# Kernel tuning notes

Hardware: AMD Instinct MI355X
Metric: run time of the kernel (lower is better)

The kernel has to match this reference:

```python
import jax, jax.numpy as jnp
import numpy as np

B, S, D = 32, 128, 1024      # encoder batch, seq len, embed_dim
C = 65536                    # nclasses (sense inventory)
N = 512                      # number of gathered WSD target tokens
NNZ = 262144                 # nnz of sparse label adjacency A (avg degree 4)
EPS = 1e-5                   # BatchNorm1d eps


def setup_inputs() -> dict:
    key = jax.random.key(0)
    ks = jax.random.split(key, 7)
    enc_out = jax.random.normal(ks[0], (B, S, D), dtype=jnp.float32)
    batch_idx = jax.random.randint(ks[1], (N,), 0, B)
    tgt = jax.random.randint(ks[2], (N,), 0, S)
    A_indices = jax.random.randint(ks[3], (2, NNZ), 0, C)
    A_values = jax.random.uniform(ks[4], (NNZ,), dtype=jnp.float32)
    wt2_w = jax.random.normal(ks[5], (C, D), dtype=jnp.float32) / np.sqrt(D).astype(np.float32)
    wt2_b = jax.random.normal(ks[6], (C,), dtype=jnp.float32) * 0.02
    return {"enc_out": enc_out, "wt2_w": wt2_w, "wt2_b": wt2_b,
            "A_values": A_values, "batch_idx": batch_idx, "tgt": tgt,
            "A_indices": A_indices}


def reference(enc_out, wt2_w, wt2_b, A_values, batch_idx, tgt, A_indices):
    # gather target-token embeddings: [N, D]
    g = enc_out[batch_idx, tgt]
    # BatchNorm1d(affine=False), training mode -> batch stats, biased var
    mean = jnp.mean(g, axis=0)
    var = jnp.var(g, axis=0)
    h0 = (g - mean) / jnp.sqrt(var + EPS)
    # wt2 Linear + swish -> logits over classes Z: [N, C]
    h1 = jax.nn.swish(h0 @ wt2_w.T + wt2_b)
    # sparse spmm: torch_sparse.spmm(ii, vv, m=C, n=C, matrix=Z.T).T == Z @ A.T
    row, col = A_indices[0], A_indices[1]
    gathered = h1.T[col] * A_values[:, None]            # [NNZ, N]
    neighbors = jax.ops.segment_sum(gathered, row, num_segments=C).T  # [N, C]
    # residual add (renormalize=False)
    return neighbors + h1
```

## Files before the change

### kernel.cpp

```cpp
#include <hip/hip_runtime.h>
#include <hip/hip_bf16.h>

typedef unsigned short u16;
typedef unsigned int   u32;
typedef __attribute__((ext_vector_type(8))) short bf16x8;
typedef __attribute__((ext_vector_type(4))) float f32x4;

static constexpr int kS = 128, kD = 1024, kC = 65536, kN = 512, kNNZ = 262144;

__device__ __forceinline__ u16 f2bf(float x) {
  u32 u = __float_as_uint(x);
  u32 r = (u + 0x7fffu + ((u >> 16) & 1u)) >> 16;
  return (u16)r;
}
__device__ __forceinline__ u32 pack2(float a, float b) {
  return (u32)f2bf(a) | ((u32)f2bf(b) << 16);
}
__device__ __forceinline__ float bf_lo(u32 v) { return __uint_as_float(v << 16); }
__device__ __forceinline__ float bf_hi(u32 v) { return __uint_as_float(v & 0xffff0000u); }

__global__ void k_bn_part(const float* __restrict__ enc, const int* __restrict__ bidx,
                          const int* __restrict__ tgt, float* __restrict__ part) {
  __shared__ int offs[64];
  int n0 = blockIdx.y * 64;
  if (threadIdx.x < 64) offs[threadIdx.x] = bidx[n0 + threadIdx.x] * kS + tgt[n0 + threadIdx.x];
  __syncthreads();
  int d = blockIdx.x * 256 + threadIdx.x;
  float s = 0.f, ss = 0.f;
  for (int i = 0; i < 64; ++i) {
    float v = enc[(size_t)offs[i] * kD + d];
    s += v; ss += v * v;
  }
  part[(blockIdx.y * 2 + 0) * kD + d] = s;
  part[(blockIdx.y * 2 + 1) * kD + d] = ss;
}

__global__ void k_bn_fin(const float* __restrict__ part, float* __restrict__ mean,
                         float* __restrict__ rstd) {
  int d = blockIdx.x * 256 + threadIdx.x;
  float s = 0.f, ss = 0.f;
#pragma unroll
  for (int b = 0; b < 8; ++b) {
    s  += part[(b * 2 + 0) * kD + d];
    ss += part[(b * 2 + 1) * kD + d];
  }
  float m = s * (1.f / kN);
  float var = ss * (1.f / kN) - m * m;
  mean[d] = m;
  rstd[d] = 1.f / sqrtf(var + 1e-5f);
}

__global__ void k_bn_apply(const float* __restrict__ enc, const int* __restrict__ bidx,
                           const int* __restrict__ tgt, const float* __restrict__ mean,
                           const float* __restrict__ rstd, u16* __restrict__ h0) {
  int i = blockIdx.x * blockDim.x + threadIdx.x;
  int n = i >> 8;
  int d = (i & 255) << 2;
  size_t src = (size_t)(bidx[n] * kS + tgt[n]) * kD + d;
  float4 v  = *(const float4*)(enc + src);
  float4 mn = *(const float4*)(mean + d);
  float4 rs = *(const float4*)(rstd + d);
  u32 q0 = pack2((v.x - mn.x) * rs.x, (v.y - mn.y) * rs.y);
  u32 q1 = pack2((v.z - mn.z) * rs.z, (v.w - mn.w) * rs.w);
  *(uint2*)(h0 + (size_t)n * kD + d) = make_uint2(q0, q1);
}

__global__ void k_hist(const int* __restrict__ rows, int* __restrict__ hist) {
  int e = blockIdx.x * blockDim.x + threadIdx.x;
  if (e < kNNZ) atomicAdd(&hist[rows[e]], 1);
}

__global__ __launch_bounds__(1024) void k_scan(int* __restrict__ hist, int* __restrict__ cursor) {
  __shared__ int sm[1024];
  int t = threadIdx.x;
  int base = t * 64;
  int sum = 0;
  for (int i = 0; i < 64; ++i) sum += hist[base + i];
  sm[t] = sum;
  __syncthreads();
  for (int off = 1; off < 1024; off <<= 1) {
    int v = (t >= off) ? sm[t - off] : 0;
    __syncthreads();
    sm[t] += v;
    __syncthreads();
  }
  int run = sm[t] - sum;
  for (int i = 0; i < 64; ++i) {
    int v = hist[base + i];
    hist[base + i] = run;
    cursor[base + i] = run;
    run += v;
  }
  if (t == 1023) hist[kC] = run;
}

__global__ void k_scatter(const int* __restrict__ rows, const int* __restrict__ cols,
                          const float* __restrict__ vals, int* __restrict__ cursor,
                          int* __restrict__ scol, float* __restrict__ sval) {
  int e = blockIdx.x * blockDim.x + threadIdx.x;
  if (e < kNNZ) {
    int r = rows[e];
    int p = atomicAdd(&cursor[r], 1);
    scol[p] = cols[e];
    sval[p] = vals[e];
  }
}

__global__ __launch_bounds__(512)
void k_gemm_f(const float* __restrict__ W, const u16* __restrict__ h0,
              const float* __restrict__ bias, u16* __restrict__ h1t) {
  __shared__ __align__(16) u16 Ab[128 * 40];
  __shared__ __align__(16) u16 Bb[512 * 40];
  const int t = threadIdx.x;
  const int l = t & 63, w = t >> 6;
  const int wm = (w >> 2) * 64, wn = (w & 3) * 128;
  const int cb = blockIdx.x * 128;

  const int ar = t >> 3, aq = t & 7;
  const int br = t >> 2, bq = t & 3;

  const float* gA0 = W + (size_t)(cb + ar) * kD + aq * 4;
  const float* gA1 = W + (size_t)(cb + ar + 64) * kD + aq * 4;
  const u16*   gB  = h0 + (size_t)br * kD + bq * 8;

  char* Abc = (char*)Ab;
  char* Bbc = (char*)Bb;
  u32 aw0 = ar * 80 + aq * 8, aw1 = (ar + 64) * 80 + aq * 8;
  u32 bw = br * 80 + bq * 16;

  f32x4 acc[4][8];
#pragma unroll
  for (int a = 0; a < 4; ++a)
#pragma unroll
    for (int b = 0; b < 8; ++b) acc[a][b] = (f32x4){0.f, 0.f, 0.f, 0.f};

  float4 nA0 = *(const float4*)gA0;
  float4 nA1 = *(const float4*)gA1;
  uint4 nB0 = *(const uint4*)(gB);
  uint4 nB1 = *(const uint4*)(gB + 128 * kD);
  uint4 nB2 = *(const uint4*)(gB + 256 * kD);
  uint4 nB3 = *(const uint4*)(gB + 384 * kD);

#pragma unroll 1
  for (int it = 0; it < 32; ++it) {
    *(uint2*)(Abc + aw0) = make_uint2(pack2(nA0.x, nA0.y), pack2(nA0.z, nA0.w));
    *(uint2*)(Abc + aw1) = make_uint2(pack2(nA1.x, nA1.y), pack2(nA1.z, nA1.w));
    *(uint4*)(Bbc + bw)  = nB0;
    *(uint4*)(Bbc + bw + 128 * 80) = nB1;
    *(uint4*)(Bbc + bw + 256 * 80) = nB2;
    *(uint4*)(Bbc + bw + 384 * 80) = nB3;
    int ktn = (it < 31) ? (it + 1) * 32 : 0;
    nA0 = *(const float4*)(gA0 + ktn);
    nA1 = *(const float4*)(gA1 + ktn);
    nB0 = *(const uint4*)(gB + ktn);
    nB1 = *(const uint4*)(gB + 128 * kD + ktn);
    nB2 = *(const uint4*)(gB + 256 * kD + ktn);
    nB3 = *(const uint4*)(gB + 384 * kD + ktn);
    asm volatile("s_waitcnt lgkmcnt(0)" ::: "memory");
    __builtin_amdgcn_s_barrier();
    __builtin_amdgcn_sched_barrier(0);
    bf16x8 af[4], bv[8];
#pragma unroll
    for (int mb = 0; mb < 4; ++mb)
      af[mb] = *(const bf16x8*)(Abc + (wm + mb * 16 + (l & 15)) * 80 + (l >> 4) * 16);
#pragma unroll
    for (int nb = 0; nb < 8; ++nb)
      bv[nb] = *(const bf16x8*)(Bbc + (wn + nb * 16 + (l & 15)) * 80 + (l >> 4) * 16);
#pragma unroll
    for (int mb = 0; mb < 4; ++mb)
#pragma unroll
      for (int nb = 0; nb < 8; ++nb)
        acc[mb][nb] = __builtin_amdgcn_mfma_f32_16x16x32_bf16(af[mb], bv[nb], acc[mb][nb], 0, 0, 0);
    asm volatile("s_waitcnt lgkmcnt(0)" ::: "memory");
    __builtin_amdgcn_s_barrier();
    __builtin_amdgcn_sched_barrier(0);
  }

#pragma unroll
  for (int mb = 0; mb < 4; ++mb) {
    int rb = wm + mb * 16 + (l >> 4) * 4;
#pragma unroll
    for (int i = 0; i < 4; ++i) {
      int c = cb + rb + i;
      float bvs = bias[c];
#pragma unroll
      for (int nb = 0; nb < 8; ++nb) {
        float x = acc[mb][nb][i] + bvs;
        float sw = x / (1.f + __expf(-x));
        h1t[(size_t)c * kN + (wn + nb * 16 + (l & 15))] = f2bf(sw);
      }
    }
  }
}

__global__ __launch_bounds__(512)
void k_spmm(const u16* __restrict__ h1t, const int* __restrict__ rowptr,
            const int* __restrict__ scol, const float* __restrict__ sval,
            float* __restrict__ out) {
  __shared__ float tile[32 * 512];
  int r0 = blockIdx.x * 32;
  int t = threadIdx.x, w = t >> 6, l = t & 63;
#pragma unroll
  for (int j = 0; j < 4; ++j) {
    int rl = w * 4 + j;
    int r = r0 + rl;
    uint4 hv = ((const uint4*)(h1t + (size_t)r * kN))[l];
    float a0 = bf_lo(hv.x), a1 = bf_hi(hv.x), a2 = bf_lo(hv.y), a3 = bf_hi(hv.y);
    float a4 = bf_lo(hv.z), a5 = bf_hi(hv.z), a6 = bf_lo(hv.w), a7 = bf_hi(hv.w);
    int e0 = rowptr[r], e1 = rowptr[r + 1];
    int c = 0; float v = 0.f;
    if (e0 < e1) { c = scol[e0]; v = sval[e0]; }
    for (int e = e0; e < e1; ++e) {
      uint4 cv = ((const uint4*)(h1t + (size_t)c * kN))[l];
      int cn = 0; float vn = 0.f;
      if (e + 1 < e1) { cn = scol[e + 1]; vn = sval[e + 1]; }
      a0 = fmaf(v, bf_lo(cv.x), a0); a1 = fmaf(v, bf_hi(cv.x), a1);
      a2 = fmaf(v, bf_lo(cv.y), a2); a3 = fmaf(v, bf_hi(cv.y), a3);
      a4 = fmaf(v, bf_lo(cv.z), a4); a5 = fmaf(v, bf_hi(cv.z), a5);
      a6 = fmaf(v, bf_lo(cv.w), a6); a7 = fmaf(v, bf_hi(cv.w), a7);
      c = cn; v = vn;
    }
    int sw = (rl & 7) << 2;
    *(float4*)&tile[rl * 512 + ((8 * l) ^ sw)]     = make_float4(a0, a1, a2, a3);
    *(float4*)&tile[rl * 512 + ((8 * l + 4) ^ sw)] = make_float4(a4, a5, a6, a7);
  }
  __syncthreads();
  int r = l & 31;
  int swr = (r & 7) << 2;
#pragma unroll
  for (int it = 0; it < 32; ++it) {
    int n = it * 16 + w * 2 + (l >> 5);
    out[(size_t)n * kC + r0 + r] = tile[r * 512 + (n ^ swr)];
  }
}

extern "C" void kernel_launch(void* const* d_in, const int* in_sizes, int n_in,
                              void* d_out, int out_size, void* d_ws, size_t ws_size,
                              hipStream_t stream) {
  (void)in_sizes; (void)n_in; (void)out_size; (void)ws_size;
  const float* enc   = (const float*)d_in[0];
  const float* W     = (const float*)d_in[1];
  const float* bias  = (const float*)d_in[2];
  const float* Avals = (const float*)d_in[3];
  const int*   bidx  = (const int*)d_in[4];
  const int*   tgt   = (const int*)d_in[5];
  const int*   Arow  = (const int*)d_in[6];
  const int*   Acol  = Arow + kNNZ;
  float* out = (float*)d_out;

  char* ws = (char*)d_ws;
  float* mean   = (float*)(ws);
  float* rstd   = (float*)(ws + 4096);
  u16*   h0     = (u16*)  (ws + 8192);
  int*   rowptr = (int*)  (ws + 1056768);
  int*   cursor = (int*)  (ws + 1319168);
  int*   scol   = (int*)  (ws + 1581312);
  float* sval   = (float*)(ws + 2629888);
  float* part   = (float*)(ws + 3678464);
  u16*   h1t    = (u16*)  (ws + 4194304);

  hipMemsetAsync(rowptr, 0, (kC + 1) * sizeof(int), stream);
  k_bn_part<<<dim3(4, 8), 256, 0, stream>>>(enc, bidx, tgt, part);
  k_bn_fin<<<4, 256, 0, stream>>>(part, mean, rstd);
  k_bn_apply<<<512, 256, 0, stream>>>(enc, bidx, tgt, mean, rstd, h0);
  k_hist<<<kNNZ / 256, 256, 0, stream>>>(Arow, rowptr);
  k_scan<<<1, 1024, 0, stream>>>(rowptr, cursor);
  k_scatter<<<kNNZ / 256, 256, 0, stream>>>(Arow, Acol, Avals, cursor, scol, sval);
  k_gemm_f<<<kC / 128, 512, 0, stream>>>(W, h0, bias, h1t);
  k_spmm<<<kC / 32, 512, 0, stream>>>(h1t, rowptr, scol, sval, out);
}
```

Measured before the change: 293.9 us.

## Pre-pack activations in MFMA fragment layout and load B operand directly from global

The BN apply kernel now writes the normalized activations in a k-group-major packed layout, so each lane of the GEMM can load its B-operand MFMA fragment straight from global memory into registers instead of staging it through LDS. The GEMM moves to 1024 threads with a 2x8 wave grid of 64x64 tiles and double-buffers the small W tile in LDS across alternating k-steps. This cuts LDS traffic and LDS footprint. In exchange every wave re-reads B from global or L2, and the larger block raises register pressure.

```diff
diff --git a/kernel.cpp b/kernel.cpp
--- a/kernel.cpp
+++ b/kernel.cpp
@@ -50,19 +50,25 @@
   rstd[d] = 1.f / sqrtf(var + 1e-5f);
 }
 
-__global__ void k_bn_apply(const float* __restrict__ enc, const int* __restrict__ bidx,
-                           const int* __restrict__ tgt, const float* __restrict__ mean,
-                           const float* __restrict__ rstd, u16* __restrict__ h0) {
-  int i = blockIdx.x * blockDim.x + threadIdx.x;
-  int n = i >> 8;
-  int d = (i & 255) << 2;
-  size_t src = (size_t)(bidx[n] * kS + tgt[n]) * kD + d;
-  float4 v  = *(const float4*)(enc + src);
-  float4 mn = *(const float4*)(mean + d);
-  float4 rs = *(const float4*)(rstd + d);
-  u32 q0 = pack2((v.x - mn.x) * rs.x, (v.y - mn.y) * rs.y);
-  u32 q1 = pack2((v.z - mn.z) * rs.z, (v.w - mn.w) * rs.w);
-  *(uint2*)(h0 + (size_t)n * kD + d) = make_uint2(q0, q1);
+__global__ void k_bn_pack(const float* __restrict__ enc, const int* __restrict__ bidx,
+                          const int* __restrict__ tgt, const float* __restrict__ mean,
+                          const float* __restrict__ rstd, u16* __restrict__ Bp) {
+  int i = blockIdx.x * 256 + threadIdx.x;
+  int n = i & 511;
+  int g = i >> 9;
+  int k0 = g * 8;
+  size_t src = (size_t)(bidx[n] * kS + tgt[n]) * kD + k0;
+  float4 v0 = *(const float4*)(enc + src);
+  float4 v1 = *(const float4*)(enc + src + 4);
+  float4 m0 = *(const float4*)(mean + k0);
+  float4 m1 = *(const float4*)(mean + k0 + 4);
+  float4 r0 = *(const float4*)(rstd + k0);
+  float4 r1 = *(const float4*)(rstd + k0 + 4);
+  u32 q0 = pack2((v0.x - m0.x) * r0.x, (v0.y - m0.y) * r0.y);
+  u32 q1 = pack2((v0.z - m0.z) * r0.z, (v0.w - m0.w) * r0.w);
+  u32 q2 = pack2((v1.x - m1.x) * r1.x, (v1.y - m1.y) * r1.y);
+  u32 q3 = pack2((v1.z - m1.z) * r1.z, (v1.w - m1.w) * r1.w);
+  *(uint4*)(Bp + (size_t)i * 8) = make_uint4(q0, q1, q2, q3);
 }
 
 __global__ void k_hist(const int* __restrict__ rows, int* __restrict__ hist) {
@@ -106,88 +112,97 @@
   }
 }
 
-__global__ __launch_bounds__(512)
-void k_gemm_f(const float* __restrict__ W, const u16* __restrict__ h0,
-              const float* __restrict__ bias, u16* __restrict__ h1t) {
-  __shared__ __align__(16) u16 Ab[128 * 40];
-  __shared__ __align__(16) u16 Bb[512 * 40];
+__global__ __launch_bounds__(1024)
+void k_gemm_f2(const float* __restrict__ W, const u16* __restrict__ Bp,
+               const float* __restrict__ bias, u16* __restrict__ h1t) {
+  __shared__ __align__(16) u16 Ab0[128 * 36];
+  __shared__ __align__(16) u16 Ab1[128 * 36];
   const int t = threadIdx.x;
-  const int l = t & 63, w = t >> 6;
-  const int wm = (w >> 2) * 64, wn = (w & 3) * 128;
+  const int l = t & 63;
+  const int w = t >> 6;
+  const int wm = (w >> 3) * 64, wn = (w & 7) * 64;
   const int cb = blockIdx.x * 128;
-
   const int ar = t >> 3, aq = t & 7;
-  const int br = t >> 2, bq = t & 3;
-
-  const float* gA0 = W + (size_t)(cb + ar) * kD + aq * 4;
-  const float* gA1 = W + (size_t)(cb + ar + 64) * kD + aq * 4;
-  const u16*   gB  = h0 + (size_t)br * kD + bq * 8;
-
-  char* Abc = (char*)Ab;
-  char* Bbc = (char*)Bb;
-  u32 aw0 = ar * 80 + aq * 8, aw1 = (ar + 64) * 80 + aq * 8;
-  u32 bw = br * 80 + bq * 16;
-
-  f32x4 acc[4][8];
+  const int q = l >> 4, ln = l & 15;
+  const float* gA = W + (size_t)(cb + ar) * kD + aq * 4;
+  u16* awp0 = Ab0 + ar * 36 + aq * 4;
+  u16* awp1 = Ab1 + ar * 36 + aq * 4;
+  const u16* gB = Bp + ((size_t)q * 512 + wn + ln) * 8;
+
+  f32x4 acc[4][4];
 #pragma unroll
   for (int a = 0; a < 4; ++a)
 #pragma unroll
-    for (int b = 0; b < 8; ++b) acc[a][b] = (f32x4){0.f, 0.f, 0.f, 0.f};
-
-  float4 nA0 = *(const float4*)gA0;
-  float4 nA1 = *(const float4*)gA1;
-  uint4 nB0 = *(const uint4*)(gB);
-  uint4 nB1 = *(const uint4*)(gB + 128 * kD);
-  uint4 nB2 = *(const uint4*)(gB + 256 * kD);
-  uint4 nB3 = *(const uint4*)(gB + 384 * kD);
+    for (int b = 0; b < 4; ++b) acc[a][b] = (f32x4){0.f, 0.f, 0.f, 0.f};
+
+  float4 fA;
+  bf16x8 bvA[4], bvB[4];
+
+  fA = *(const float4*)(gA);
+#pragma unroll
+  for (int nb = 0; nb < 4; ++nb) bvA[nb] = *(const bf16x8*)(gB + nb * 128);
+  *(uint2*)awp0 = make_uint2(pack2(fA.x, fA.y), pack2(fA.z, fA.w));
+  fA = *(const float4*)(gA + 32);
+#pragma unroll
+  for (int nb = 0; nb < 4; ++nb) bvB[nb] = *(const bf16x8*)(gB + 16384 + nb * 128);
+  asm volatile("s_waitcnt lgkmcnt(0)" ::: "memory");
+  __builtin_amdgcn_s_barrier();
+  __builtin_amdgcn_sched_barrier(0);
 
 #pragma unroll 1
-  for (int it = 0; it < 32; ++it) {
-    *(uint2*)(Abc + aw0) = make_uint2(pack2(nA0.x, nA0.y), pack2(nA0.z, nA0.w));
-    *(uint2*)(Abc + aw1) = make_uint2(pack2(nA1.x, nA1.y), pack2(nA1.z, nA1.w));
-    *(uint4*)(Bbc + bw)  = nB0;
-    *(uint4*)(Bbc + bw + 128 * 80) = nB1;
-    *(uint4*)(Bbc + bw + 256 * 80) = nB2;
-    *(uint4*)(Bbc + bw + 384 * 80) = nB3;
-    int ktn = (it < 31) ? (it + 1) * 32 : 0;
-    nA0 = *(const float4*)(gA0 + ktn);
-    nA1 = *(const float4*)(gA1 + ktn);
-    nB0 = *(const uint4*)(gB + ktn);
-    nB1 = *(const uint4*)(gB + 128 * kD + ktn);
-    nB2 = *(const uint4*)(gB + 256 * kD + ktn);
-    nB3 = *(const uint4*)(gB + 384 * kD + ktn);
-    asm volatile("s_waitcnt lgkmcnt(0)" ::: "memory");
-    __builtin_amdgcn_s_barrier();
-    __builtin_amdgcn_sched_barrier(0);
-    bf16x8 af[4], bv[8];
-#pragma unroll
-    for (int mb = 0; mb < 4; ++mb)
-      af[mb] = *(const bf16x8*)(Abc + (wm + mb * 16 + (l & 15)) * 80 + (l >> 4) * 16);
-#pragma unroll
-    for (int nb = 0; nb < 8; ++nb)
-      bv[nb] = *(const bf16x8*)(Bbc + (wn + nb * 16 + (l & 15)) * 80 + (l >> 4) * 16);
-#pragma unroll
-    for (int mb = 0; mb < 4; ++mb)
-#pragma unroll
-      for (int nb = 0; nb < 8; ++nb)
-        acc[mb][nb] = __builtin_amdgcn_mfma_f32_16x16x32_bf16(af[mb], bv[nb], acc[mb][nb], 0, 0, 0);
-    asm volatile("s_waitcnt lgkmcnt(0)" ::: "memory");
-    __builtin_amdgcn_s_barrier();
-    __builtin_amdgcn_sched_barrier(0);
+  for (int tt = 0; tt < 16; ++tt) {
+    {
+#pragma unroll
+      for (int mb = 0; mb < 4; ++mb) {
+        bf16x8 af = *(const bf16x8*)(Ab0 + (wm + mb * 16 + ln) * 36 + q * 8);
+#pragma unroll
+        for (int nb = 0; nb < 4; ++nb)
+          acc[mb][nb] = __builtin_amdgcn_mfma_f32_16x16x32_bf16(af, bvA[nb], acc[mb][nb], 0, 0, 0);
+      }
+      *(uint2*)awp1 = make_uint2(pack2(fA.x, fA.y), pack2(fA.z, fA.w));
+      int ktn = (2 * tt + 2) & 31;
+      fA = *(const float4*)(gA + ktn * 32);
+#pragma unroll
+      for (int nb = 0; nb < 4; ++nb)
+        bvA[nb] = *(const bf16x8*)(gB + (size_t)ktn * 16384 + nb * 128);
+      asm volatile("s_waitcnt lgkmcnt(0)" ::: "memory");
+      __builtin_amdgcn_s_barrier();
+      __builtin_amdgcn_sched_barrier(0);
+    }
+    {
+#pragma unroll
+      for (int mb = 0; mb < 4; ++mb) {
+        bf16x8 af = *(const bf16x8*)(Ab1 + (wm + mb * 16 + ln) * 36 + q * 8);
+#pragma unroll
+        for (int nb = 0; nb < 4; ++nb)
+          acc[mb][nb] = __builtin_amdgcn_mfma_f32_16x16x32_bf16(af, bvB[nb], acc[mb][nb], 0, 0, 0);
+      }
+      if (tt < 15) {
+        *(uint2*)awp0 = make_uint2(pack2(fA.x, fA.y), pack2(fA.z, fA.w));
+        int ktn = 2 * tt + 3;
+        fA = *(const float4*)(gA + ktn * 32);
+#pragma unroll
+        for (int nb = 0; nb < 4; ++nb)
+          bvB[nb] = *(const bf16x8*)(gB + (size_t)ktn * 16384 + nb * 128);
+        asm volatile("s_waitcnt lgkmcnt(0)" ::: "memory");
+        __builtin_amdgcn_s_barrier();
+        __builtin_amdgcn_sched_barrier(0);
+      }
+    }
   }
 
 #pragma unroll
   for (int mb = 0; mb < 4; ++mb) {
-    int rb = wm + mb * 16 + (l >> 4) * 4;
+    int rb = wm + mb * 16 + q * 4;
 #pragma unroll
     for (int i = 0; i < 4; ++i) {
       int c = cb + rb + i;
       float bvs = bias[c];
 #pragma unroll
-      for (int nb = 0; nb < 8; ++nb) {
+      for (int nb = 0; nb < 4; ++nb) {
         float x = acc[mb][nb][i] + bvs;
         float sw = x / (1.f + __expf(-x));
-        h1t[(size_t)c * kN + (wn + nb * 16 + (l & 15))] = f2bf(sw);
+        h1t[(size_t)c * kN + (wn + nb * 16 + ln)] = f2bf(sw);
       }
     }
   }
@@ -251,7 +266,7 @@
   char* ws = (char*)d_ws;
   float* mean   = (float*)(ws);
   float* rstd   = (float*)(ws + 4096);
-  u16*   h0     = (u16*)  (ws + 8192);
+  u16*   Bp     = (u16*)  (ws + 8192);
   int*   rowptr = (int*)  (ws + 1056768);
   int*   cursor = (int*)  (ws + 1319168);
   int*   scol   = (int*)  (ws + 1581312);
@@ -262,10 +277,10 @@
   hipMemsetAsync(rowptr, 0, (kC + 1) * sizeof(int), stream);
   k_bn_part<<<dim3(4, 8), 256, 0, stream>>>(enc, bidx, tgt, part);
   k_bn_fin<<<4, 256, 0, stream>>>(part, mean, rstd);
-  k_bn_apply<<<512, 256, 0, stream>>>(enc, bidx, tgt, mean, rstd, h0);
+  k_bn_pack<<<256, 256, 0, stream>>>(enc, bidx, tgt, mean, rstd, Bp);
   k_hist<<<kNNZ / 256, 256, 0, stream>>>(Arow, rowptr);
   k_scan<<<1, 1024, 0, stream>>>(rowptr, cursor);
   k_scatter<<<kNNZ / 256, 256, 0, stream>>>(Arow, Acol, Avals, cursor, scol, sval);
-  k_gemm_f<<<kC / 128, 512, 0, stream>>>(W, h0, bias, h1t);
+  k_gemm_f2<<<kC / 128, 1024, 0, stream>>>(W, Bp, bias, h1t);
   k_spmm<<<kC / 32, 512, 0, stream>>>(h1t, rowptr, scol, sval, out);
 }
```

Measured after the change: 285.6 us. 1.03x faster.
